# Optimization experiments

Measured on AMD Instinct MI355X. Metric: run time of the kernel, lower is better.

Reference implementation:

```python
import jax, jax.numpy as jnp
import numpy as np

B, S, D = 4, 4096, 256

def setup_inputs() -> dict:
    key = jax.random.key(0)
    k1, k2 = jax.random.split(key)
    x = jax.random.normal(k1, (B, S, D), dtype=jnp.float32)
    # xavier_uniform for Linear(D, 2D): bound = sqrt(6/(fan_in+fan_out))
    bound = np.sqrt(6.0 / (D + 2 * D))
    W = jax.random.uniform(k2, (2 * D, D), dtype=jnp.float32, minval=-bound, maxval=bound)
    b = jnp.zeros((2 * D,), dtype=jnp.float32)
    return {"x": x, "W": W, "b": b}

def reference(x, W, b):
    # qk projection: [B,S,2D]
    qk = jnp.einsum('bsd,ed->bse', x, W) + b
    q, k = jnp.split(qk, 2, axis=-1)            # each [B,S,D]
    v = x
    scale = 1.0 / np.sqrt(D)
    logits = jnp.einsum('bqd,bkd->bqk', q, k) * scale   # [B,S,S]
    attn = jax.nn.softmax(logits, axis=-1)
    values = jnp.einsum('bqk,bkd->bqd', attn, v)        # [B,S,D]
    return values.sum(axis=1)                           # [B,D] sum-pool over queries
```

## Files before the change

kernel.cpp:

```cpp
#include <hip/hip_runtime.h>
#include <stdint.h>

typedef __bf16 v8bf __attribute__((ext_vector_type(8)));
typedef float  v4f  __attribute__((ext_vector_type(4)));
typedef int    v4i  __attribute__((ext_vector_type(4)));
typedef unsigned short u16;
typedef unsigned char  u8;

static constexpr int B_ = 4, S_ = 4096, D_ = 256, E_ = 512;
static constexpr float QSC_ = 127.0f / 4.8f;
static constexpr float DQ_  = 1.288045e-4f;

#define AS1C(p) ((const __attribute__((address_space(1))) void*)(p))
#define AS3(p)  ((__attribute__((address_space(3))) void*)(p))

__device__ __forceinline__ u8 f2i8(float f) {
    float t = fminf(fmaxf(f * QSC_, -127.f), 127.f);
    return (u8)(signed char)__float2int_rn(t);
}
__device__ __forceinline__ v8bf cvt8(const float* p) {
    float4 f0 = *(const float4*)p;
    float4 f1 = *(const float4*)(p + 4);
    v8bf t;
    t[0] = (__bf16)f0.x; t[1] = (__bf16)f0.y; t[2] = (__bf16)f0.z; t[3] = (__bf16)f0.w;
    t[4] = (__bf16)f1.x; t[5] = (__bf16)f1.y; t[6] = (__bf16)f1.z; t[7] = (__bf16)f1.w;
    return t;
}

__global__ __launch_bounds__(256) void k_proj(const float* __restrict__ x,
                                              const float* __restrict__ W,
                                              const float* __restrict__ bias,
                                              u8* __restrict__ Qi,
                                              u8* __restrict__ Ki) {
    const int tid = threadIdx.x, wave = tid >> 6, lane = tid & 63;
    const int l15 = lane & 15, quad = lane >> 4;
    const int tt = blockIdx.x * 2 + (wave >> 1);
    const int wsel = wave & 1;
    const int tbase = tt * 16;

    v8bf a[8];
    const float* xrow = x + (size_t)(tbase + l15) * D_ + quad * 8;
#pragma unroll
    for (int j = 0; j < 8; ++j) a[j] = cvt8(xrow + j * 32);

    u8* dst = wsel ? Ki : Qi;
    const float* wbase = W + (size_t)(wsel * 256 + l15) * D_ + quad * 8;
    const float* bb = bias + wsel * 256;

    v8bf wcur[8], wnxt[8];
#pragma unroll
    for (int j = 0; j < 8; ++j) wcur[j] = cvt8(wbase + j * 32);

    auto tile = [&](const v8bf (&wb)[8], int nt) {
        v4f acc = {0.f, 0.f, 0.f, 0.f};
#pragma unroll
        for (int j = 0; j < 8; ++j)
            acc = __builtin_amdgcn_mfma_f32_16x16x32_bf16(a[j], wb[j], acc, 0, 0, 0);
        const int col = nt * 16 + l15;
        const float bv = bb[col];
#pragma unroll
        for (int r = 0; r < 4; ++r) {
            const int tok = tbase + quad * 4 + r;
            dst[tok * D_ + col] = f2i8(acc[r] + bv);
        }
    };

    for (int nt = 0; nt < 16; nt += 2) {
        const float* wp1 = wbase + (size_t)(nt + 1) * 16 * D_;
#pragma unroll
        for (int j = 0; j < 8; ++j) wnxt[j] = cvt8(wp1 + j * 32);
        tile(wcur, nt);
        if (nt + 2 < 16) {
            const float* wp2 = wbase + (size_t)(nt + 2) * 16 * D_;
#pragma unroll
            for (int j = 0; j < 8; ++j) wcur[j] = cvt8(wp2 + j * 32);
        }
        tile(wnxt, nt + 1);
    }
}

__device__ __forceinline__ void stage64(const u8* src, u8* dst,
                                        int wave, int lane) {
#pragma unroll
    for (int v = 0; v < 4; ++v) {
        const int sbase = v * 256 + wave * 64;
        const int slot = sbase + lane;
        const int R = slot >> 4, P = slot & 15;
        const int c = P ^ (R & 15);
        __builtin_amdgcn_global_load_lds(AS1C(src + R * 256 + c * 16),
                                         AS3(dst + sbase * 16), 16, 0, 0);
    }
}

__global__ __launch_bounds__(256, 2) void k_passA(const u8* __restrict__ Qi,
                                                  const u8* __restrict__ Ki,
                                                  float* __restrict__ Zp) {
    __shared__ u8 sK[2][16384];
    const int tid = threadIdx.x, wave = tid >> 6, lane = tid & 63;
    const int l15 = lane & 15, quad = lane >> 4;
    const int blk = blockIdx.x;
    const int ks = blk & 7;
    const int qg = (blk >> 3) & 15;
    const int b = blk >> 7;
    const int qbase = qg * 256 + wave * 64;
    const int kstart = ks * 512;

    v4i a[4][4];
    {
        const u8* qp = Qi + (size_t)(b * S_ + qbase + l15) * D_ + quad * 16;
#pragma unroll
        for (int s = 0; s < 4; ++s)
#pragma unroll
            for (int c = 0; c < 4; ++c)
                a[s][c] = *(const v4i*)(qp + s * 16 * D_ + c * 64);
    }
    float z[4][4];
#pragma unroll
    for (int s = 0; s < 4; ++s)
#pragma unroll
        for (int r = 0; r < 4; ++r) z[s][r] = 0.f;

    const u8* kb = Ki + (size_t)(b * S_ + kstart) * D_;
    stage64(kb, sK[0], wave, lane);

    for (int t = 0; t < 8; ++t) {
        __syncthreads();
        if (t + 1 < 8) stage64(kb + (size_t)(t + 1) * 64 * D_, sK[(t + 1) & 1], wave, lane);
        const u8* base = sK[t & 1];
#pragma unroll
        for (int u = 0; u < 4; ++u) {
            v4i bf[4];
#pragma unroll
            for (int kc = 0; kc < 4; ++kc) {
                const int P = (kc * 4 + quad) ^ l15;
                bf[kc] = *(const v4i*)(base + (u * 16 + l15) * 256 + P * 16);
            }
            v4i c0 = {0,0,0,0}, c1 = {0,0,0,0}, c2 = {0,0,0,0}, c3 = {0,0,0,0};
#pragma unroll
            for (int kc = 0; kc < 4; ++kc) {
                c0 = __builtin_amdgcn_mfma_i32_16x16x64_i8(a[0][kc], bf[kc], c0, 0, 0, 0);
                c1 = __builtin_amdgcn_mfma_i32_16x16x64_i8(a[1][kc], bf[kc], c1, 0, 0, 0);
                c2 = __builtin_amdgcn_mfma_i32_16x16x64_i8(a[2][kc], bf[kc], c2, 0, 0, 0);
                c3 = __builtin_amdgcn_mfma_i32_16x16x64_i8(a[3][kc], bf[kc], c3, 0, 0, 0);
            }
#pragma unroll
            for (int r = 0; r < 4; ++r) {
                z[0][r] += __builtin_amdgcn_exp2f((float)c0[r] * DQ_);
                z[1][r] += __builtin_amdgcn_exp2f((float)c1[r] * DQ_);
                z[2][r] += __builtin_amdgcn_exp2f((float)c2[r] * DQ_);
                z[3][r] += __builtin_amdgcn_exp2f((float)c3[r] * DQ_);
            }
        }
    }

    float* zdst = Zp + (size_t)ks * B_ * S_ + b * S_ + qbase;
#pragma unroll
    for (int s = 0; s < 4; ++s)
#pragma unroll
        for (int r = 0; r < 4; ++r) {
            float v = z[s][r];
#pragma unroll
            for (int off = 1; off < 16; off <<= 1) v += __shfl_xor(v, off);
            if (l15 == 0) zdst[s * 16 + quad * 4 + r] = v;
        }
}

__global__ __launch_bounds__(256, 2) void k_passB(const u8* __restrict__ Qi,
                                                  const u8* __restrict__ Ki,
                                                  const float* __restrict__ Zp,
                                                  float* __restrict__ wp) {
    __shared__ u8 sQ[2][16384];
    __shared__ float sRZ[512];
    const int tid = threadIdx.x, wave = tid >> 6, lane = tid & 63;
    const int l15 = lane & 15, quad = lane >> 4;
    const int blk = blockIdx.x;
    const int qs = blk & 7;
    const int kg = (blk >> 3) & 15;
    const int b = blk >> 7;
    const int kbase = kg * 256 + wave * 64;
    const int qstart = qs * 512;

    v4i bk[4][4];
    {
        const u8* kp = Ki + (size_t)(b * S_ + kbase + l15) * D_ + quad * 16;
#pragma unroll
        for (int s = 0; s < 4; ++s)
#pragma unroll
            for (int c = 0; c < 4; ++c)
                bk[s][c] = *(const v4i*)(kp + s * 16 * D_ + c * 64);
    }
    float wsum[4] = {0.f, 0.f, 0.f, 0.f};

    const u8* qb = Qi + (size_t)(b * S_ + qstart) * D_;
    stage64(qb, sQ[0], wave, lane);

#pragma unroll
    for (int i = tid; i < 512; i += 256) {
        float zs = 0.f;
#pragma unroll
        for (int p = 0; p < 8; ++p)
            zs += Zp[(size_t)p * B_ * S_ + b * S_ + qstart + i];
        sRZ[i] = __builtin_amdgcn_rcpf(zs);
    }

    for (int t = 0; t < 8; ++t) {
        __syncthreads();
        if (t + 1 < 8) stage64(qb + (size_t)(t + 1) * 64 * D_, sQ[(t + 1) & 1], wave, lane);
        const u8* base = sQ[t & 1];
#pragma unroll
        for (int u = 0; u < 4; ++u) {
            const v4f rzv = *(const v4f*)(&sRZ[t * 64 + u * 16 + quad * 4]);
            v4i af[4];
#pragma unroll
            for (int kc = 0; kc < 4; ++kc) {
                const int P = (kc * 4 + quad) ^ l15;
                af[kc] = *(const v4i*)(base + (u * 16 + l15) * 256 + P * 16);
            }
            v4i c0 = {0,0,0,0}, c1 = {0,0,0,0}, c2 = {0,0,0,0}, c3 = {0,0,0,0};
#pragma unroll
            for (int kc = 0; kc < 4; ++kc) {
                c0 = __builtin_amdgcn_mfma_i32_16x16x64_i8(af[kc], bk[0][kc], c0, 0, 0, 0);
                c1 = __builtin_amdgcn_mfma_i32_16x16x64_i8(af[kc], bk[1][kc], c1, 0, 0, 0);
                c2 = __builtin_amdgcn_mfma_i32_16x16x64_i8(af[kc], bk[2][kc], c2, 0, 0, 0);
                c3 = __builtin_amdgcn_mfma_i32_16x16x64_i8(af[kc], bk[3][kc], c3, 0, 0, 0);
            }
            wsum[0] += __builtin_amdgcn_exp2f((float)c0[0] * DQ_) * rzv[0] + __builtin_amdgcn_exp2f((float)c0[1] * DQ_) * rzv[1]
                     + __builtin_amdgcn_exp2f((float)c0[2] * DQ_) * rzv[2] + __builtin_amdgcn_exp2f((float)c0[3] * DQ_) * rzv[3];
            wsum[1] += __builtin_amdgcn_exp2f((float)c1[0] * DQ_) * rzv[0] + __builtin_amdgcn_exp2f((float)c1[1] * DQ_) * rzv[1]
                     + __builtin_amdgcn_exp2f((float)c1[2] * DQ_) * rzv[2] + __builtin_amdgcn_exp2f((float)c1[3] * DQ_) * rzv[3];
            wsum[2] += __builtin_amdgcn_exp2f((float)c2[0] * DQ_) * rzv[0] + __builtin_amdgcn_exp2f((float)c2[1] * DQ_) * rzv[1]
                     + __builtin_amdgcn_exp2f((float)c2[2] * DQ_) * rzv[2] + __builtin_amdgcn_exp2f((float)c2[3] * DQ_) * rzv[3];
            wsum[3] += __builtin_amdgcn_exp2f((float)c3[0] * DQ_) * rzv[0] + __builtin_amdgcn_exp2f((float)c3[1] * DQ_) * rzv[1]
                     + __builtin_amdgcn_exp2f((float)c3[2] * DQ_) * rzv[2] + __builtin_amdgcn_exp2f((float)c3[3] * DQ_) * rzv[3];
        }
    }

    float* wdst = wp + (size_t)qs * B_ * S_ + b * S_ + kbase;
#pragma unroll
    for (int s = 0; s < 4; ++s) {
        wsum[s] += __shfl_xor(wsum[s], 16);
        wsum[s] += __shfl_xor(wsum[s], 32);
        if (quad == 0) wdst[s * 16 + l15] = wsum[s];
    }
}

__global__ __launch_bounds__(256) void k_final(const float* __restrict__ x,
                                               const float* __restrict__ wp,
                                               float* __restrict__ out) {
    const int b = blockIdx.x >> 5, kc = blockIdx.x & 31;
    const int d = threadIdx.x;
    const int k0 = kc * 128;
    float acc = 0.f;
    const float* xp = x + (size_t)(b * S_ + k0) * D_ + d;
#pragma unroll 4
    for (int kk = 0; kk < 128; ++kk) {
        float wk = 0.f;
#pragma unroll
        for (int p = 0; p < 8; ++p)
            wk += wp[(size_t)p * B_ * S_ + b * S_ + k0 + kk];
        acc += wk * xp[(size_t)kk * D_];
    }
    atomicAdd(&out[b * D_ + d], acc);
}

extern "C" void kernel_launch(void* const* d_in, const int* in_sizes, int n_in,
                              void* d_out, int out_size, void* d_ws, size_t ws_size,
                              hipStream_t stream) {
    const float* x    = (const float*)d_in[0];
    const float* W    = (const float*)d_in[1];
    const float* bias = (const float*)d_in[2];
    float* out = (float*)d_out;

    char* ws = (char*)d_ws;
    u8*    Qi = (u8*)ws;
    u8*    Ki = Qi + (size_t)B_ * S_ * D_;
    float* Zp = (float*)(ws + 8388608);
    float* wp = Zp + 8 * B_ * S_;

    hipMemsetAsync(out, 0, B_ * D_ * sizeof(float), stream);
    k_proj <<<512, 256, 0, stream>>>(x, W, bias, Qi, Ki);
    k_passA<<<512, 256, 0, stream>>>(Qi, Ki, Zp);
    k_passB<<<512, 256, 0, stream>>>(Qi, Ki, Zp, wp);
    k_final<<<128, 256, 0, stream>>>(x, wp, out);
}
```

Before: 191.9 us.

## Pre-convert W to bf16 and stage 128-row tiles in attention passes

A new small kernel converts W to bf16 once per call, so the projection kernel loads bf16 fragments directly instead of loading fp32 and converting in every block. Separately, passA and passB now stage 128 rows per LDS buffer instead of 64, which halves the number of barrier iterations. The cost is a doubled LDS footprint (64KB per block), which may reduce occupancy under launch_bounds(256,2), plus one extra kernel launch.

Result: faster. 175.0 us (-8.9%).

```diff
diff --git a/kernel.cpp b/kernel.cpp
--- a/kernel.cpp
+++ b/kernel.cpp
@@ -14,21 +14,24 @@
 #define AS1C(p) ((const __attribute__((address_space(1))) void*)(p))
 #define AS3(p)  ((__attribute__((address_space(3))) void*)(p))
 
+__device__ __forceinline__ v8bf ldfrag(const u16* p) {
+    return __builtin_bit_cast(v8bf, *(const uint4*)p);
+}
+__device__ __forceinline__ u16 f2bf(float f) {
+    return __builtin_bit_cast(u16, (__bf16)f);
+}
 __device__ __forceinline__ u8 f2i8(float f) {
     float t = fminf(fmaxf(f * QSC_, -127.f), 127.f);
     return (u8)(signed char)__float2int_rn(t);
 }
-__device__ __forceinline__ v8bf cvt8(const float* p) {
-    float4 f0 = *(const float4*)p;
-    float4 f1 = *(const float4*)(p + 4);
-    v8bf t;
-    t[0] = (__bf16)f0.x; t[1] = (__bf16)f0.y; t[2] = (__bf16)f0.z; t[3] = (__bf16)f0.w;
-    t[4] = (__bf16)f1.x; t[5] = (__bf16)f1.y; t[6] = (__bf16)f1.z; t[7] = (__bf16)f1.w;
-    return t;
+
+__global__ void k_convw(const float* __restrict__ Wf, u16* __restrict__ Wb) {
+    int i = blockIdx.x * 256 + threadIdx.x;
+    Wb[i] = f2bf(Wf[i]);
 }
 
 __global__ __launch_bounds__(256) void k_proj(const float* __restrict__ x,
-                                              const float* __restrict__ W,
+                                              const u16* __restrict__ Wb,
                                               const float* __restrict__ bias,
                                               u8* __restrict__ Qi,
                                               u8* __restrict__ Ki) {
@@ -41,15 +44,22 @@
     v8bf a[8];
     const float* xrow = x + (size_t)(tbase + l15) * D_ + quad * 8;
 #pragma unroll
-    for (int j = 0; j < 8; ++j) a[j] = cvt8(xrow + j * 32);
+    for (int j = 0; j < 8; ++j) {
+        float4 f0 = *(const float4*)(xrow + j * 32);
+        float4 f1 = *(const float4*)(xrow + j * 32 + 4);
+        v8bf t;
+        t[0] = (__bf16)f0.x; t[1] = (__bf16)f0.y; t[2] = (__bf16)f0.z; t[3] = (__bf16)f0.w;
+        t[4] = (__bf16)f1.x; t[5] = (__bf16)f1.y; t[6] = (__bf16)f1.z; t[7] = (__bf16)f1.w;
+        a[j] = t;
+    }
 
     u8* dst = wsel ? Ki : Qi;
-    const float* wbase = W + (size_t)(wsel * 256 + l15) * D_ + quad * 8;
+    const u16* wbase = Wb + (size_t)(wsel * 256 + l15) * D_ + quad * 8;
     const float* bb = bias + wsel * 256;
 
     v8bf wcur[8], wnxt[8];
 #pragma unroll
-    for (int j = 0; j < 8; ++j) wcur[j] = cvt8(wbase + j * 32);
+    for (int j = 0; j < 8; ++j) wcur[j] = ldfrag(wbase + j * 32);
 
     auto tile = [&](const v8bf (&wb)[8], int nt) {
         v4f acc = {0.f, 0.f, 0.f, 0.f};
@@ -66,23 +76,23 @@
     };
 
     for (int nt = 0; nt < 16; nt += 2) {
-        const float* wp1 = wbase + (size_t)(nt + 1) * 16 * D_;
-#pragma unroll
-        for (int j = 0; j < 8; ++j) wnxt[j] = cvt8(wp1 + j * 32);
+        const u16* wp1 = wbase + (size_t)(nt + 1) * 16 * D_;
+#pragma unroll
+        for (int j = 0; j < 8; ++j) wnxt[j] = ldfrag(wp1 + j * 32);
         tile(wcur, nt);
         if (nt + 2 < 16) {
-            const float* wp2 = wbase + (size_t)(nt + 2) * 16 * D_;
-#pragma unroll
-            for (int j = 0; j < 8; ++j) wcur[j] = cvt8(wp2 + j * 32);
+            const u16* wp2 = wbase + (size_t)(nt + 2) * 16 * D_;
+#pragma unroll
+            for (int j = 0; j < 8; ++j) wcur[j] = ldfrag(wp2 + j * 32);
         }
         tile(wnxt, nt + 1);
     }
 }
 
-__device__ __forceinline__ void stage64(const u8* src, u8* dst,
-                                        int wave, int lane) {
-#pragma unroll
-    for (int v = 0; v < 4; ++v) {
+__device__ __forceinline__ void stage128(const u8* src, u8* dst,
+                                         int wave, int lane) {
+#pragma unroll
+    for (int v = 0; v < 8; ++v) {
         const int sbase = v * 256 + wave * 64;
         const int slot = sbase + lane;
         const int R = slot >> 4, P = slot & 15;
@@ -95,7 +105,7 @@
 __global__ __launch_bounds__(256, 2) void k_passA(const u8* __restrict__ Qi,
                                                   const u8* __restrict__ Ki,
                                                   float* __restrict__ Zp) {
-    __shared__ u8 sK[2][16384];
+    __shared__ u8 sK[2][32768];
     const int tid = threadIdx.x, wave = tid >> 6, lane = tid & 63;
     const int l15 = lane & 15, quad = lane >> 4;
     const int blk = blockIdx.x;
@@ -121,14 +131,14 @@
         for (int r = 0; r < 4; ++r) z[s][r] = 0.f;
 
     const u8* kb = Ki + (size_t)(b * S_ + kstart) * D_;
-    stage64(kb, sK[0], wave, lane);
-
-    for (int t = 0; t < 8; ++t) {
+    stage128(kb, sK[0], wave, lane);
+
+    for (int t = 0; t < 4; ++t) {
         __syncthreads();
-        if (t + 1 < 8) stage64(kb + (size_t)(t + 1) * 64 * D_, sK[(t + 1) & 1], wave, lane);
+        if (t + 1 < 4) stage128(kb + (size_t)(t + 1) * 128 * D_, sK[(t + 1) & 1], wave, lane);
         const u8* base = sK[t & 1];
 #pragma unroll
-        for (int u = 0; u < 4; ++u) {
+        for (int u = 0; u < 8; ++u) {
             v4i bf[4];
 #pragma unroll
             for (int kc = 0; kc < 4; ++kc) {
@@ -169,7 +179,7 @@
                                                   const u8* __restrict__ Ki,
                                                   const float* __restrict__ Zp,
                                                   float* __restrict__ wp) {
-    __shared__ u8 sQ[2][16384];
+    __shared__ u8 sQ[2][32768];
     __shared__ float sRZ[512];
     const int tid = threadIdx.x, wave = tid >> 6, lane = tid & 63;
     const int l15 = lane & 15, quad = lane >> 4;
@@ -192,7 +202,7 @@
     float wsum[4] = {0.f, 0.f, 0.f, 0.f};
 
     const u8* qb = Qi + (size_t)(b * S_ + qstart) * D_;
-    stage64(qb, sQ[0], wave, lane);
+    stage128(qb, sQ[0], wave, lane);
 
 #pragma unroll
     for (int i = tid; i < 512; i += 256) {
@@ -203,13 +213,13 @@
         sRZ[i] = __builtin_amdgcn_rcpf(zs);
     }
 
-    for (int t = 0; t < 8; ++t) {
+    for (int t = 0; t < 4; ++t) {
         __syncthreads();
-        if (t + 1 < 8) stage64(qb + (size_t)(t + 1) * 64 * D_, sQ[(t + 1) & 1], wave, lane);
+        if (t + 1 < 4) stage128(qb + (size_t)(t + 1) * 128 * D_, sQ[(t + 1) & 1], wave, lane);
         const u8* base = sQ[t & 1];
 #pragma unroll
-        for (int u = 0; u < 4; ++u) {
-            const v4f rzv = *(const v4f*)(&sRZ[t * 64 + u * 16 + quad * 4]);
+        for (int u = 0; u < 8; ++u) {
+            const v4f rzv = *(const v4f*)(&sRZ[t * 128 + u * 16 + quad * 4]);
             v4i af[4];
 #pragma unroll
             for (int kc = 0; kc < 4; ++kc) {
@@ -276,9 +286,11 @@
     u8*    Ki = Qi + (size_t)B_ * S_ * D_;
     float* Zp = (float*)(ws + 8388608);
     float* wp = Zp + 8 * B_ * S_;
+    u16*   Wb = (u16*)(wp + 8 * B_ * S_);
 
     hipMemsetAsync(out, 0, B_ * D_ * sizeof(float), stream);
-    k_proj <<<512, 256, 0, stream>>>(x, W, bias, Qi, Ki);
+    k_convw<<<E_ * D_ / 256, 256, 0, stream>>>(W, Wb);
+    k_proj <<<512, 256, 0, stream>>>(x, Wb, bias, Qi, Ki);
     k_passA<<<512, 256, 0, stream>>>(Qi, Ki, Zp);
     k_passB<<<512, 256, 0, stream>>>(Qi, Ki, Zp, wp);
     k_final<<<128, 256, 0, stream>>>(x, wp, out);
```
